# Kernel tuning notes

Measured on AMD Instinct MI355X. Metric: run time of the kernel, lower is better.

## Reference

```python
import jax, jax.numpy as jnp
import numpy as np

T, D, H = 8192, 128, 1024  # seq_len, obs_dim, lstm_hidden_size


def setup_inputs() -> dict:
    key = jax.random.key(0)
    ks = jax.random.split(key, 9)
    lim = 1.0 / np.sqrt(H)  # eqx LSTMCell/Linear uniform init scale

    def u(k, shape):
        return jax.random.uniform(k, shape, minval=-lim, maxval=lim, dtype=jnp.float32)

    obs = jax.random.normal(ks[0], (T, D), dtype=jnp.float32)
    W_ih0 = u(ks[1], (4 * H, D))
    W_hh0 = u(ks[2], (4 * H, H))
    b0 = u(ks[3], (4 * H,))
    W_ih1 = u(ks[4], (4 * H, H))
    W_hh1 = u(ks[5], (4 * H, H))
    b1 = u(ks[6], (4 * H,))
    W_dec = u(ks[7], (2 * D, H))
    b_dec = u(ks[8], (2 * D,))
    return {"obs": obs, "W_ih0": W_ih0, "W_hh0": W_hh0, "b0": b0,
            "W_ih1": W_ih1, "W_hh1": W_hh1, "b1": b1,
            "W_dec": W_dec, "b_dec": b_dec}


def _lstm_cell(gx, h, c, W_hh):
    # gx: (4H,) precomputed input projection + bias; h, c: (H,)
    z = gx + W_hh @ h
    i, f, g, o = jnp.split(z, 4)
    i = jax.nn.sigmoid(i)
    f = jax.nn.sigmoid(f)
    g = jnp.tanh(g)
    o = jax.nn.sigmoid(o)
    c_new = f * c + i * g
    h_new = o * jnp.tanh(c_new)
    return h_new, c_new


def reference(obs, W_ih0, W_hh0, b0, W_ih1, W_hh1, b1, W_dec, b_dec):
    d = obs.shape[1]
    hdim = W_hh0.shape[1]
    # teacher forcing: input at step t is obs[t-1], obs[-1] replaced by zeros
    shifted = jnp.concatenate([jnp.zeros((1, d), obs.dtype), obs[:-1]], axis=0)
    # layer-0 input projection is input-only -> precompute as one big GEMM (T, 4H)
    gx0_all = shifted @ W_ih0.T + b0

    def step(state, gx0_t):
        (h0, c0), (h1, c1) = state
        h0, c0 = _lstm_cell(gx0_t, h0, c0, W_hh0)
        gx1 = W_ih1 @ h0 + b1
        h1, c1 = _lstm_cell(gx1, h1, c1, W_hh1)
        return ((h0, c0), (h1, c1)), h1

    z = jnp.zeros((hdim,), obs.dtype)
    init = ((z, z), (z, z))
    _, all_h = jax.lax.scan(step, init, gx0_all)  # all_h: (T, H)

    params = all_h @ W_dec.T + b_dec  # (T, 2D)
    loc = params[:, :d]
    scale = jax.nn.softplus(params[:, d:]) + 1e-4
    return loc, scale
```

## Files before the change

### kernel.cpp

```cpp
#include <hip/hip_runtime.h>
#include <math.h>

#define TT 8192
#define DD 128
#define HH 1024
#define RINGN 64
#define NA 64
#define NB 128
#define NWG (NA + NB)


typedef unsigned long long ull;

__device__ __forceinline__ ull ldpair(const ull* p) {
  return __hip_atomic_load(p, __ATOMIC_RELAXED, __HIP_MEMORY_SCOPE_AGENT);
}
__device__ __forceinline__ void stpair(ull* p, float v, unsigned e) {
  ull u = ((ull)e << 32) | (ull)__float_as_uint(v);
  __hip_atomic_store(p, u, __ATOMIC_RELAXED, __HIP_MEMORY_SCOPE_AGENT);
}
__device__ __forceinline__ unsigned ldflag(const unsigned* p) {
  return __hip_atomic_load(p, __ATOMIC_RELAXED, __HIP_MEMORY_SCOPE_AGENT);
}
__device__ __forceinline__ void stflag(unsigned* p, unsigned v) {
  __hip_atomic_store(p, v, __ATOMIC_RELAXED, __HIP_MEMORY_SCOPE_AGENT);
}
__device__ __forceinline__ float sigm(float x) { return 1.0f / (1.0f + expf(-x)); }
__device__ __forceinline__ float softplusf(float x) {
  return x > 0.0f ? x + log1pf(expf(-x)) : log1pf(expf(x));
}

#define DRAIN()  asm volatile("s_waitcnt vmcnt(0)" ::: "memory")
#define CFENCE() asm volatile("" ::: "memory")

#define FMA16(W)                                                      \
  a0 = fmaf(W[0][4*i+0], h4.x, a0); a0 = fmaf(W[0][4*i+1], h4.y, a0); \
  a0 = fmaf(W[0][4*i+2], h4.z, a0); a0 = fmaf(W[0][4*i+3], h4.w, a0); \
  a1 = fmaf(W[1][4*i+0], h4.x, a1); a1 = fmaf(W[1][4*i+1], h4.y, a1); \
  a1 = fmaf(W[1][4*i+2], h4.z, a1); a1 = fmaf(W[1][4*i+3], h4.w, a1); \
  a2 = fmaf(W[2][4*i+0], h4.x, a2); a2 = fmaf(W[2][4*i+1], h4.y, a2); \
  a2 = fmaf(W[2][4*i+2], h4.z, a2); a2 = fmaf(W[2][4*i+3], h4.w, a2); \
  a3 = fmaf(W[3][4*i+0], h4.x, a3); a3 = fmaf(W[3][4*i+1], h4.y, a3); \
  a3 = fmaf(W[3][4*i+2], h4.z, a3); a3 = fmaf(W[3][4*i+3], h4.w, a3);

__global__ void __launch_bounds__(512, 1) deepar_persistent(
    const float* __restrict__ obs,
    const float* __restrict__ Wih0, const float* __restrict__ Whh0, const float* __restrict__ b0,
    const float* __restrict__ Wih1, const float* __restrict__ Whh1, const float* __restrict__ b1,
    const float* __restrict__ Wdec, const float* __restrict__ bdec,
    float* __restrict__ out,
    unsigned* b_cons, unsigned* a_fA, unsigned* a_fB, unsigned* b_fB,
    ull* h0A, ull* h0B, ull* h1B)
{
  __shared__ __align__(16) float hx[2][2304];

  const int wg   = blockIdx.x;
  const int tid  = threadIdx.x;
  const int wid  = tid >> 6;
  const int lane = tid & 63;

  if (wg < NA) {
    const int rg = tid >> 5;
    const int q  = tid & 31;
    const int j  = wg * 16 + rg;
    const int k0 = q * 36;
    float w[4][36];
    #pragma unroll
    for (int i = 0; i < 9; ++i) {
      const int kb = k0 + 4 * i;
      #pragma unroll
      for (int r = 0; r < 4; ++r) {
        const float* src = (kb < HH) ? (Whh0 + (size_t)(r * HH + j) * HH + kb)
                                     : (Wih0 + (size_t)(r * HH + j) * DD + (kb - HH));
        const float4 v = *(const float4*)src;
        w[r][4*i+0] = v.x; w[r][4*i+1] = v.y; w[r][4*i+2] = v.z; w[r][4*i+3] = v.w;
      }
    }
    float bs[4];
    #pragma unroll
    for (int r = 0; r < 4; ++r) bs[r] = b0[r * HH + j];
    float creg = 0.0f;

    for (int t = 0; t < TT; ++t) {
      float a0 = 0.f, a1 = 0.f, a2 = 0.f, a3 = 0.f;
      if (t > 0) {
        const float* obr = obs + (size_t)(t - 1) * DD;
        #pragma unroll
        for (int i = 0; i < 9; ++i) {
          const int kb = k0 + 4 * i;
          if (kb >= HH) { const float4 h4 = *(const float4*)(obr + (kb - HH)); FMA16(w) }
        }
      }
      if (wid == 1 && ((t & 15) == 0) && t >= 48) {
        const unsigned need = (unsigned)(t - 32);
        while (!__all((ldflag(&b_cons[lane]) >= need) &
                      (ldflag(&b_cons[lane + 64]) >= need))) {}
      }
      if (wid == 0 && t > 0) {
        const unsigned tg = (unsigned)t;
        while (!__all((lane == wg) | (ldflag(&a_fA[lane]) >= tg))) {}
      }
      __builtin_amdgcn_s_barrier();
      float* Lb = hx[t & 1];
      if (t > 0) {
        const ull* sl = h0A + (size_t)((t - 1) & (RINGN - 1)) * HH;
        const unsigned ee = (unsigned)t;
        ull u0 = ldpair(sl + tid);
        ull u1 = ldpair(sl + tid + 512);
        while ((unsigned)(u0 >> 32) != ee) u0 = ldpair(sl + tid);
        Lb[tid] = __uint_as_float((unsigned)u0);
        while ((unsigned)(u1 >> 32) != ee) u1 = ldpair(sl + tid + 512);
        Lb[tid + 512] = __uint_as_float((unsigned)u1);
      }
      __syncthreads();
      if (t > 0) {
        #pragma unroll
        for (int i = 0; i < 9; ++i) {
          const int kb = k0 + 4 * i;
          if (kb < HH) { const float4 h4 = *(const float4*)&Lb[kb]; FMA16(w) }
        }
      }
      #pragma unroll
      for (int s = 1; s < 32; s <<= 1) {
        a0 += __shfl_xor(a0, s); a1 += __shfl_xor(a1, s);
        a2 += __shfl_xor(a2, s); a3 += __shfl_xor(a3, s);
      }
      if (q == 0) {
        const float ig = sigm(a0 + bs[0]);
        const float fg = sigm(a1 + bs[1]);
        const float gg = tanhf(a2 + bs[2]);
        const float og = sigm(a3 + bs[3]);
        creg = fg * creg + ig * gg;
        const float hv = og * tanhf(creg);
        const size_t off = (size_t)(t & (RINGN - 1)) * HH + j;
        const unsigned ep = (unsigned)(t + 1);
        stpair(&h0A[off], hv, ep);
        stpair(&h0B[off], hv, ep);
      }
      DRAIN();
      __builtin_amdgcn_s_barrier();
      CFENCE();
      if (tid == 0) { stflag(&a_fA[wg], (unsigned)(t + 1));
                      stflag(&a_fB[wg], (unsigned)(t + 1)); }
    }

  } else {
    const int rg = tid >> 6;
    const int q  = tid & 63;
    const int s_ = wg - NA;
    const int j  = s_ * 8 + rg;
    const int k0 = q * 32;
    float w[4][32];
    #pragma unroll
    for (int i = 0; i < 8; ++i) {
      const int kb = k0 + 4 * i;
      #pragma unroll
      for (int r = 0; r < 4; ++r) {
        const float* src = (kb < HH) ? (Wih1 + (size_t)(r * HH + j) * HH + kb)
                                     : (Whh1 + (size_t)(r * HH + j) * HH + (kb - HH));
        const float4 v = *(const float4*)src;
        w[r][4*i+0] = v.x; w[r][4*i+1] = v.y; w[r][4*i+2] = v.z; w[r][4*i+3] = v.w;
      }
    }
    float bs[4];
    #pragma unroll
    for (int r = 0; r < 4; ++r) bs[r] = b1[r * HH + j];
    float creg = 0.0f;
    const int p0 = tid + 4 * (tid >> 5);
    const int p1 = p0 + 576;
    const int p2 = p0 + 1152;
    const int p3 = p2 + 576;
    const int baseB = (q < 32) ? q * 36 : 1152 + (q - 32) * 36;
    const int crow = s_ * 2 + (wid - 2);
    float wd[16];
    float bsd = 0.0f;
    if (wid == 2 || wid == 3) {
      #pragma unroll
      for (int i = 0; i < 4; ++i) {
        const float4 v = *(const float4*)(Wdec + (size_t)crow * HH + lane * 16 + 4 * i);
        wd[4*i+0] = v.x; wd[4*i+1] = v.y; wd[4*i+2] = v.z; wd[4*i+3] = v.w;
      }
      bsd = bdec[crow];
    }
    const int dbase = 1152 + lane * 16 + 4 * ((lane * 16) >> 5);

    for (int t = 0; t <= TT; ++t) {
      if (wid == 0) {
        const unsigned eA = (unsigned)(t + 1);
        const unsigned eB = (unsigned)t;
        for (;;) {
          int ok = 1;
          if (t < TT) ok &= (ldflag(&a_fB[lane]) >= eA);
          if (t > 0) {
            ok &= (lane == s_)        | (ldflag(&b_fB[lane])      >= eB);
            ok &= ((lane + 64) == s_) | (ldflag(&b_fB[lane + 64]) >= eB);
          }
          if (__all(ok)) break;
        }
      }
      __builtin_amdgcn_s_barrier();
      float* Lb = hx[t & 1];
      {
        const unsigned e0 = (unsigned)(t + 1);
        const unsigned e1 = (unsigned)t;
        if (t < TT) {
          const ull* s0 = h0B + (size_t)(t & (RINGN - 1)) * HH;
          ull u0 = ldpair(s0 + tid);
          ull u1 = ldpair(s0 + tid + 512);
          while ((unsigned)(u0 >> 32) != e0) u0 = ldpair(s0 + tid);
          Lb[p0] = __uint_as_float((unsigned)u0);
          while ((unsigned)(u1 >> 32) != e0) u1 = ldpair(s0 + tid + 512);
          Lb[p1] = __uint_as_float((unsigned)u1);
        }
        const ull* s1 = h1B + (size_t)((t - 1) & (RINGN - 1)) * HH;
        ull u2 = ldpair(s1 + tid);
        ull u3 = ldpair(s1 + tid + 512);
        while ((unsigned)(u2 >> 32) != e1) u2 = ldpair(s1 + tid);
        Lb[p2] = __uint_as_float((unsigned)u2);
        while ((unsigned)(u3 >> 32) != e1) u3 = ldpair(s1 + tid + 512);
        Lb[p3] = __uint_as_float((unsigned)u3);
      }
      __syncthreads();
      if (tid == 64 && t < TT) stflag(&b_cons[s_], (unsigned)(t + 1));
      if (t < TT) {
        float a0 = 0.f, a1 = 0.f, a2 = 0.f, a3 = 0.f;
        #pragma unroll
        for (int i = 0; i < 8; ++i) {
          const float4 h4 = *(const float4*)&Lb[baseB + 4 * i];
          FMA16(w)
        }
        #pragma unroll
        for (int s = 1; s < 64; s <<= 1) {
          a0 += __shfl_xor(a0, s); a1 += __shfl_xor(a1, s);
          a2 += __shfl_xor(a2, s); a3 += __shfl_xor(a3, s);
        }
        if (q == 0) {
          const float ig = sigm(a0 + bs[0]);
          const float fg = sigm(a1 + bs[1]);
          const float gg = tanhf(a2 + bs[2]);
          const float og = sigm(a3 + bs[3]);
          creg = fg * creg + ig * gg;
          stpair(&h1B[(size_t)(t & (RINGN - 1)) * HH + j], og * tanhf(creg),
                 (unsigned)(t + 1));
        }
        DRAIN();
        __builtin_amdgcn_s_barrier();
        CFENCE();
        if (tid == 0) stflag(&b_fB[s_], (unsigned)(t + 1));
      }
      if (t > 0 && (wid == 2 || wid == 3)) {
        float a = 0.f;
        #pragma unroll
        for (int i = 0; i < 4; ++i) {
          const float4 h4 = *(const float4*)&Lb[dbase + 4 * i];
          a = fmaf(wd[4*i+0], h4.x, a); a = fmaf(wd[4*i+1], h4.y, a);
          a = fmaf(wd[4*i+2], h4.z, a); a = fmaf(wd[4*i+3], h4.w, a);
        }
        #pragma unroll
        for (int s = 1; s < 64; s <<= 1) a += __shfl_xor(a, s);
        if (lane == 0) {
          const float z = a + bsd;
          if (crow < DD) out[(size_t)(t - 1) * DD + crow] = z;
          else out[(size_t)TT * DD + (size_t)(t - 1) * DD + (crow - DD)]
                 = softplusf(z) + 1e-4f;
        }
      }
    }
  }
}

extern "C" void kernel_launch(void* const* d_in, const int* in_sizes, int n_in,
                              void* d_out, int out_size, void* d_ws, size_t ws_size,
                              hipStream_t stream) {
  const float* obs  = (const float*)d_in[0];
  const float* Wih0 = (const float*)d_in[1];
  const float* Whh0 = (const float*)d_in[2];
  const float* b0   = (const float*)d_in[3];
  const float* Wih1 = (const float*)d_in[4];
  const float* Whh1 = (const float*)d_in[5];
  const float* b1   = (const float*)d_in[6];
  const float* Wdec = (const float*)d_in[7];
  const float* bdec = (const float*)d_in[8];
  float* out = (float*)d_out;

  const size_t RB = (size_t)RINGN * HH * 8;
  unsigned char* ws = (unsigned char*)d_ws;
  unsigned* b_cons = (unsigned*)(ws);
  unsigned* a_fA   = (unsigned*)(ws + 1024);
  unsigned* a_fB   = (unsigned*)(ws + 1536);
  unsigned* b_fB   = (unsigned*)(ws + 2048);
  ull* h0A = (ull*)(ws + 4096);
  ull* h0B = (ull*)(ws + 4096 + RB);
  ull* h1B = (ull*)(ws + 4096 + 2 * RB);

  hipMemsetAsync(ws, 0, 4096 + 3 * RB, stream);

  hipLaunchKernelGGL(deepar_persistent, dim3(NWG), dim3(512), 0, stream,
                     obs, Wih0, Whh0, b0, Wih1, Whh1, b1, Wdec, bdec, out,
                     b_cons, a_fA, a_fB, b_fB, h0A, h0B, h1B);
}
```

Measured before the change: 34.40 ms.

## Replace per-step flag barriers with epoch-tagged ring polling by a single wave

Drops the per-workgroup completion flags (a_fA, a_fB, b_fB) and the drain-plus-barrier that published them. Consumers now rely only on the epoch tags stored with each h value. One wave per workgroup sweeps the whole 1024-entry ring slot with 16 outstanding loads per lane and re-polls only the entries that are still stale. Layer-0 wave 0 defers its obs contribution until after the LDS barrier so the poll starts sooner. This removes a flag round-trip and a vmcnt drain from the recurrent critical path, but concentrates the polling traffic in one wave and leans on the per-element epoch checks alone for correctness.

```diff
diff --git a/kernel.cpp b/kernel.cpp
--- a/kernel.cpp
+++ b/kernel.cpp
@@ -30,8 +30,31 @@
   return x > 0.0f ? x + log1pf(expf(-x)) : log1pf(expf(x));
 }
 
-#define DRAIN()  asm volatile("s_waitcnt vmcnt(0)" ::: "memory")
-#define CFENCE() asm volatile("" ::: "memory")
+template<int PAD>
+__device__ __forceinline__ void sweep_ring(const ull* sl, unsigned ee,
+                                           float* lds, int lane) {
+  ull v[16];
+  #pragma unroll
+  for (int k = 0; k < 16; ++k) v[k] = ldpair(sl + lane + 64 * k);
+  unsigned pend = 0xFFFFu;
+  for (;;) {
+    unsigned np = 0u;
+    #pragma unroll
+    for (int k = 0; k < 16; ++k) {
+      if (pend & (1u << k)) {
+        if ((unsigned)(v[k] >> 32) == ee) {
+          const int m = lane + 64 * k;
+          lds[PAD ? (m + 4 * (m >> 5)) : m] = __uint_as_float((unsigned)v[k]);
+        } else np |= (1u << k);
+      }
+    }
+    if (!np) break;
+    pend = np;
+    #pragma unroll
+    for (int k = 0; k < 16; ++k)
+      if (pend & (1u << k)) v[k] = ldpair(sl + lane + 64 * k);
+  }
+}
 
 #define FMA16(W)                                                      \
   a0 = fmaf(W[0][4*i+0], h4.x, a0); a0 = fmaf(W[0][4*i+1], h4.y, a0); \
@@ -49,8 +72,7 @@
     const float* __restrict__ Wih1, const float* __restrict__ Whh1, const float* __restrict__ b1,
     const float* __restrict__ Wdec, const float* __restrict__ bdec,
     float* __restrict__ out,
-    unsigned* b_cons, unsigned* a_fA, unsigned* a_fB, unsigned* b_fB,
-    ull* h0A, ull* h0B, ull* h1B)
+    unsigned* b_cons, ull* h0A, ull* h0B, ull* h1B)
 {
   __shared__ __align__(16) float hx[2][2304];
 
@@ -83,7 +105,7 @@
 
     for (int t = 0; t < TT; ++t) {
       float a0 = 0.f, a1 = 0.f, a2 = 0.f, a3 = 0.f;
-      if (t > 0) {
+      if (wid != 0 && t > 0) {
         const float* obr = obs + (size_t)(t - 1) * DD;
         #pragma unroll
         for (int i = 0; i < 9; ++i) {
@@ -91,29 +113,25 @@
           if (kb >= HH) { const float4 h4 = *(const float4*)(obr + (kb - HH)); FMA16(w) }
         }
       }
-      if (wid == 1 && ((t & 15) == 0) && t >= 48) {
+      if (wid == 2 && ((t & 15) == 0) && t >= 48) {
         const unsigned need = (unsigned)(t - 32);
         while (!__all((ldflag(&b_cons[lane]) >= need) &
                       (ldflag(&b_cons[lane + 64]) >= need))) {}
       }
-      if (wid == 0 && t > 0) {
-        const unsigned tg = (unsigned)t;
-        while (!__all((lane == wg) | (ldflag(&a_fA[lane]) >= tg))) {}
-      }
-      __builtin_amdgcn_s_barrier();
       float* Lb = hx[t & 1];
-      if (t > 0) {
-        const ull* sl = h0A + (size_t)((t - 1) & (RINGN - 1)) * HH;
-        const unsigned ee = (unsigned)t;
-        ull u0 = ldpair(sl + tid);
-        ull u1 = ldpair(sl + tid + 512);
-        while ((unsigned)(u0 >> 32) != ee) u0 = ldpair(sl + tid);
-        Lb[tid] = __uint_as_float((unsigned)u0);
-        while ((unsigned)(u1 >> 32) != ee) u1 = ldpair(sl + tid + 512);
-        Lb[tid + 512] = __uint_as_float((unsigned)u1);
-      }
+      if (wid == 0 && t > 0)
+        sweep_ring<0>(h0A + (size_t)((t - 1) & (RINGN - 1)) * HH,
+                      (unsigned)t, Lb, lane);
       __syncthreads();
       if (t > 0) {
+        if (wid == 0) {
+          const float* obr = obs + (size_t)(t - 1) * DD;
+          #pragma unroll
+          for (int i = 0; i < 9; ++i) {
+            const int kb = k0 + 4 * i;
+            if (kb >= HH) { const float4 h4 = *(const float4*)(obr + (kb - HH)); FMA16(w) }
+          }
+        }
         #pragma unroll
         for (int i = 0; i < 9; ++i) {
           const int kb = k0 + 4 * i;
@@ -137,11 +155,6 @@
         stpair(&h0A[off], hv, ep);
         stpair(&h0B[off], hv, ep);
       }
-      DRAIN();
-      __builtin_amdgcn_s_barrier();
-      CFENCE();
-      if (tid == 0) { stflag(&a_fA[wg], (unsigned)(t + 1));
-                      stflag(&a_fB[wg], (unsigned)(t + 1)); }
     }
 
   } else {
@@ -166,62 +179,27 @@
     #pragma unroll
     for (int r = 0; r < 4; ++r) bs[r] = b1[r * HH + j];
     float creg = 0.0f;
-    const int p0 = tid + 4 * (tid >> 5);
-    const int p1 = p0 + 576;
-    const int p2 = p0 + 1152;
-    const int p3 = p2 + 576;
     const int baseB = (q < 32) ? q * 36 : 1152 + (q - 32) * 36;
     const int crow = s_ * 2 + (wid - 2);
     float wd[16];
     float bsd = 0.0f;
     if (wid == 2 || wid == 3) {
       #pragma unroll
-      for (int i = 0; i < 4; ++i) {
-        const float4 v = *(const float4*)(Wdec + (size_t)crow * HH + lane * 16 + 4 * i);
-        wd[4*i+0] = v.x; wd[4*i+1] = v.y; wd[4*i+2] = v.z; wd[4*i+3] = v.w;
-      }
+      for (int k = 0; k < 16; ++k)
+        wd[k] = Wdec[(size_t)crow * HH + lane + 64 * k];
       bsd = bdec[crow];
     }
-    const int dbase = 1152 + lane * 16 + 4 * ((lane * 16) >> 5);
 
     for (int t = 0; t <= TT; ++t) {
-      if (wid == 0) {
-        const unsigned eA = (unsigned)(t + 1);
-        const unsigned eB = (unsigned)t;
-        for (;;) {
-          int ok = 1;
-          if (t < TT) ok &= (ldflag(&a_fB[lane]) >= eA);
-          if (t > 0) {
-            ok &= (lane == s_)        | (ldflag(&b_fB[lane])      >= eB);
-            ok &= ((lane + 64) == s_) | (ldflag(&b_fB[lane + 64]) >= eB);
-          }
-          if (__all(ok)) break;
-        }
-      }
-      __builtin_amdgcn_s_barrier();
       float* Lb = hx[t & 1];
-      {
-        const unsigned e0 = (unsigned)(t + 1);
-        const unsigned e1 = (unsigned)t;
-        if (t < TT) {
-          const ull* s0 = h0B + (size_t)(t & (RINGN - 1)) * HH;
-          ull u0 = ldpair(s0 + tid);
-          ull u1 = ldpair(s0 + tid + 512);
-          while ((unsigned)(u0 >> 32) != e0) u0 = ldpair(s0 + tid);
-          Lb[p0] = __uint_as_float((unsigned)u0);
-          while ((unsigned)(u1 >> 32) != e0) u1 = ldpair(s0 + tid + 512);
-          Lb[p1] = __uint_as_float((unsigned)u1);
-        }
-        const ull* s1 = h1B + (size_t)((t - 1) & (RINGN - 1)) * HH;
-        ull u2 = ldpair(s1 + tid);
-        ull u3 = ldpair(s1 + tid + 512);
-        while ((unsigned)(u2 >> 32) != e1) u2 = ldpair(s1 + tid);
-        Lb[p2] = __uint_as_float((unsigned)u2);
-        while ((unsigned)(u3 >> 32) != e1) u3 = ldpair(s1 + tid + 512);
-        Lb[p3] = __uint_as_float((unsigned)u3);
-      }
+      if (wid == 0)
+        sweep_ring<1>(h1B + (size_t)((t - 1) & (RINGN - 1)) * HH,
+                      (unsigned)t, Lb + 1152, lane);
+      if (wid == 1 && t < TT)
+        sweep_ring<1>(h0B + (size_t)(t & (RINGN - 1)) * HH,
+                      (unsigned)(t + 1), Lb, lane);
       __syncthreads();
-      if (tid == 64 && t < TT) stflag(&b_cons[s_], (unsigned)(t + 1));
+      if (tid == 256 && t < TT) stflag(&b_cons[s_], (unsigned)(t + 1));
       if (t < TT) {
         float a0 = 0.f, a1 = 0.f, a2 = 0.f, a3 = 0.f;
         #pragma unroll
@@ -243,18 +221,13 @@
           stpair(&h1B[(size_t)(t & (RINGN - 1)) * HH + j], og * tanhf(creg),
                  (unsigned)(t + 1));
         }
-        DRAIN();
-        __builtin_amdgcn_s_barrier();
-        CFENCE();
-        if (tid == 0) stflag(&b_fB[s_], (unsigned)(t + 1));
       }
       if (t > 0 && (wid == 2 || wid == 3)) {
         float a = 0.f;
         #pragma unroll
-        for (int i = 0; i < 4; ++i) {
-          const float4 h4 = *(const float4*)&Lb[dbase + 4 * i];
-          a = fmaf(wd[4*i+0], h4.x, a); a = fmaf(wd[4*i+1], h4.y, a);
-          a = fmaf(wd[4*i+2], h4.z, a); a = fmaf(wd[4*i+3], h4.w, a);
+        for (int k = 0; k < 16; ++k) {
+          const int m = lane + 64 * k;
+          a = fmaf(wd[k], Lb[1152 + m + 4 * (m >> 5)], a);
         }
         #pragma unroll
         for (int s = 1; s < 64; s <<= 1) a += __shfl_xor(a, s);
@@ -286,9 +259,6 @@
   const size_t RB = (size_t)RINGN * HH * 8;
   unsigned char* ws = (unsigned char*)d_ws;
   unsigned* b_cons = (unsigned*)(ws);
-  unsigned* a_fA   = (unsigned*)(ws + 1024);
-  unsigned* a_fB   = (unsigned*)(ws + 1536);
-  unsigned* b_fB   = (unsigned*)(ws + 2048);
   ull* h0A = (ull*)(ws + 4096);
   ull* h0B = (ull*)(ws + 4096 + RB);
   ull* h1B = (ull*)(ws + 4096 + 2 * RB);
@@ -297,5 +267,5 @@
 
   hipLaunchKernelGGL(deepar_persistent, dim3(NWG), dim3(512), 0, stream,
                      obs, Wih0, Whh0, b0, Wih1, Whh1, b1, Wdec, bdec, out,
-                     b_cons, a_fA, a_fB, b_fB, h0A, h0B, h1B);
-}
+                     b_cons, h0A, h0B, h1B);
+}
```

Result: slower. 55.86 ms (+62.4%).

## Drop per-step flag barriers, replicate hidden-state rings across eight copies

Applied to the files above, without the earlier changes.

Removes the per-workgroup completion flags and the drain-plus-barrier handshake. Consumers now wait only on the epoch-tagged value pairs, so each step needs no separate flag round trip. Each h value is written to eight replicated ring buffers so readers spread across copies instead of contending on one, and the ring depth drops to 32 with a tighter backpressure window. The decoder weight layout changes to a lane-strided form. The risks are an eightfold increase in store traffic per step and a narrower margin against ring wraparound.

```diff
diff --git a/kernel.cpp b/kernel.cpp
--- a/kernel.cpp
+++ b/kernel.cpp
@@ -4,10 +4,12 @@
 #define TT 8192
 #define DD 128
 #define HH 1024
-#define RINGN 64
+#define RINGN 32
+#define NREP 8
 #define NA 64
 #define NB 128
 #define NWG (NA + NB)
+#define RSTRIDE ((size_t)RINGN * HH)
 
 
 typedef unsigned long long ull;
@@ -15,8 +17,7 @@
 __device__ __forceinline__ ull ldpair(const ull* p) {
   return __hip_atomic_load(p, __ATOMIC_RELAXED, __HIP_MEMORY_SCOPE_AGENT);
 }
-__device__ __forceinline__ void stpair(ull* p, float v, unsigned e) {
-  ull u = ((ull)e << 32) | (ull)__float_as_uint(v);
+__device__ __forceinline__ void stpair(ull* p, ull u) {
   __hip_atomic_store(p, u, __ATOMIC_RELAXED, __HIP_MEMORY_SCOPE_AGENT);
 }
 __device__ __forceinline__ unsigned ldflag(const unsigned* p) {
@@ -29,9 +30,6 @@
 __device__ __forceinline__ float softplusf(float x) {
   return x > 0.0f ? x + log1pf(expf(-x)) : log1pf(expf(x));
 }
-
-#define DRAIN()  asm volatile("s_waitcnt vmcnt(0)" ::: "memory")
-#define CFENCE() asm volatile("" ::: "memory")
 
 #define FMA16(W)                                                      \
   a0 = fmaf(W[0][4*i+0], h4.x, a0); a0 = fmaf(W[0][4*i+1], h4.y, a0); \
@@ -49,8 +47,7 @@
     const float* __restrict__ Wih1, const float* __restrict__ Whh1, const float* __restrict__ b1,
     const float* __restrict__ Wdec, const float* __restrict__ bdec,
     float* __restrict__ out,
-    unsigned* b_cons, unsigned* a_fA, unsigned* a_fB, unsigned* b_fB,
-    ull* h0A, ull* h0B, ull* h1B)
+    unsigned* b_cons, ull* h0R, ull* h1R)
 {
   __shared__ __align__(16) float hx[2][2304];
 
@@ -80,33 +77,27 @@
     #pragma unroll
     for (int r = 0; r < 4; ++r) bs[r] = b0[r * HH + j];
     float creg = 0.0f;
+    const ull* myrep = h0R + (size_t)(wg & 7) * RSTRIDE;
 
     for (int t = 0; t < TT; ++t) {
+      if (wid == 2 && ((t & 7) == 0) && t >= 24) {
+        const unsigned need = (unsigned)(t - 16);
+        while (!__all((ldflag(&b_cons[lane]) >= need) &
+                      (ldflag(&b_cons[lane + 64]) >= need))) {}
+      }
       float a0 = 0.f, a1 = 0.f, a2 = 0.f, a3 = 0.f;
+      float* Lb = hx[t & 1];
       if (t > 0) {
+        const ull* sl = myrep + (size_t)((t - 1) & (RINGN - 1)) * HH;
+        ull u0 = ldpair(sl + tid);
+        ull u1 = ldpair(sl + tid + 512);
         const float* obr = obs + (size_t)(t - 1) * DD;
         #pragma unroll
         for (int i = 0; i < 9; ++i) {
           const int kb = k0 + 4 * i;
           if (kb >= HH) { const float4 h4 = *(const float4*)(obr + (kb - HH)); FMA16(w) }
         }
-      }
-      if (wid == 1 && ((t & 15) == 0) && t >= 48) {
-        const unsigned need = (unsigned)(t - 32);
-        while (!__all((ldflag(&b_cons[lane]) >= need) &
-                      (ldflag(&b_cons[lane + 64]) >= need))) {}
-      }
-      if (wid == 0 && t > 0) {
-        const unsigned tg = (unsigned)t;
-        while (!__all((lane == wg) | (ldflag(&a_fA[lane]) >= tg))) {}
-      }
-      __builtin_amdgcn_s_barrier();
-      float* Lb = hx[t & 1];
-      if (t > 0) {
-        const ull* sl = h0A + (size_t)((t - 1) & (RINGN - 1)) * HH;
         const unsigned ee = (unsigned)t;
-        ull u0 = ldpair(sl + tid);
-        ull u1 = ldpair(sl + tid + 512);
         while ((unsigned)(u0 >> 32) != ee) u0 = ldpair(sl + tid);
         Lb[tid] = __uint_as_float((unsigned)u0);
         while ((unsigned)(u1 >> 32) != ee) u1 = ldpair(sl + tid + 512);
@@ -133,15 +124,11 @@
         creg = fg * creg + ig * gg;
         const float hv = og * tanhf(creg);
         const size_t off = (size_t)(t & (RINGN - 1)) * HH + j;
-        const unsigned ep = (unsigned)(t + 1);
-        stpair(&h0A[off], hv, ep);
-        stpair(&h0B[off], hv, ep);
-      }
-      DRAIN();
-      __builtin_amdgcn_s_barrier();
-      CFENCE();
-      if (tid == 0) { stflag(&a_fA[wg], (unsigned)(t + 1));
-                      stflag(&a_fB[wg], (unsigned)(t + 1)); }
+        const ull u = ((ull)(unsigned)(t + 1) << 32) | (ull)__float_as_uint(hv);
+        #pragma unroll
+        for (int r = 0; r < NREP; ++r)
+          stpair(h0R + (size_t)r * RSTRIDE + off, u);
+      }
     }
 
   } else {
@@ -171,40 +158,28 @@
     const int p2 = p0 + 1152;
     const int p3 = p2 + 576;
     const int baseB = (q < 32) ? q * 36 : 1152 + (q - 32) * 36;
+    const ull* rep0 = h0R + (size_t)(s_ & 7) * RSTRIDE;
+    const ull* rep1 = h1R + (size_t)(s_ & 7) * RSTRIDE;
     const int crow = s_ * 2 + (wid - 2);
     float wd[16];
     float bsd = 0.0f;
     if (wid == 2 || wid == 3) {
       #pragma unroll
-      for (int i = 0; i < 4; ++i) {
-        const float4 v = *(const float4*)(Wdec + (size_t)crow * HH + lane * 16 + 4 * i);
-        wd[4*i+0] = v.x; wd[4*i+1] = v.y; wd[4*i+2] = v.z; wd[4*i+3] = v.w;
-      }
+      for (int k = 0; k < 16; ++k)
+        wd[k] = Wdec[(size_t)crow * HH + lane + 64 * k];
       bsd = bdec[crow];
     }
-    const int dbase = 1152 + lane * 16 + 4 * ((lane * 16) >> 5);
 
     for (int t = 0; t <= TT; ++t) {
-      if (wid == 0) {
-        const unsigned eA = (unsigned)(t + 1);
-        const unsigned eB = (unsigned)t;
-        for (;;) {
-          int ok = 1;
-          if (t < TT) ok &= (ldflag(&a_fB[lane]) >= eA);
-          if (t > 0) {
-            ok &= (lane == s_)        | (ldflag(&b_fB[lane])      >= eB);
-            ok &= ((lane + 64) == s_) | (ldflag(&b_fB[lane + 64]) >= eB);
-          }
-          if (__all(ok)) break;
-        }
-      }
-      __builtin_amdgcn_s_barrier();
       float* Lb = hx[t & 1];
       {
         const unsigned e0 = (unsigned)(t + 1);
         const unsigned e1 = (unsigned)t;
+        const ull* s1 = rep1 + (size_t)((t - 1) & (RINGN - 1)) * HH;
+        ull u2 = ldpair(s1 + tid);
+        ull u3 = ldpair(s1 + tid + 512);
         if (t < TT) {
-          const ull* s0 = h0B + (size_t)(t & (RINGN - 1)) * HH;
+          const ull* s0 = rep0 + (size_t)(t & (RINGN - 1)) * HH;
           ull u0 = ldpair(s0 + tid);
           ull u1 = ldpair(s0 + tid + 512);
           while ((unsigned)(u0 >> 32) != e0) u0 = ldpair(s0 + tid);
@@ -212,16 +187,13 @@
           while ((unsigned)(u1 >> 32) != e0) u1 = ldpair(s0 + tid + 512);
           Lb[p1] = __uint_as_float((unsigned)u1);
         }
-        const ull* s1 = h1B + (size_t)((t - 1) & (RINGN - 1)) * HH;
-        ull u2 = ldpair(s1 + tid);
-        ull u3 = ldpair(s1 + tid + 512);
         while ((unsigned)(u2 >> 32) != e1) u2 = ldpair(s1 + tid);
         Lb[p2] = __uint_as_float((unsigned)u2);
         while ((unsigned)(u3 >> 32) != e1) u3 = ldpair(s1 + tid + 512);
         Lb[p3] = __uint_as_float((unsigned)u3);
       }
       __syncthreads();
-      if (tid == 64 && t < TT) stflag(&b_cons[s_], (unsigned)(t + 1));
+      if (tid == 256 && t < TT) stflag(&b_cons[s_], (unsigned)(t + 1));
       if (t < TT) {
         float a0 = 0.f, a1 = 0.f, a2 = 0.f, a3 = 0.f;
         #pragma unroll
@@ -240,21 +212,20 @@
           const float gg = tanhf(a2 + bs[2]);
           const float og = sigm(a3 + bs[3]);
           creg = fg * creg + ig * gg;
-          stpair(&h1B[(size_t)(t & (RINGN - 1)) * HH + j], og * tanhf(creg),
-                 (unsigned)(t + 1));
-        }
-        DRAIN();
-        __builtin_amdgcn_s_barrier();
-        CFENCE();
-        if (tid == 0) stflag(&b_fB[s_], (unsigned)(t + 1));
+          const float hv = og * tanhf(creg);
+          const size_t off = (size_t)(t & (RINGN - 1)) * HH + j;
+          const ull u = ((ull)(unsigned)(t + 1) << 32) | (ull)__float_as_uint(hv);
+          #pragma unroll
+          for (int r = 0; r < NREP; ++r)
+            stpair(h1R + (size_t)r * RSTRIDE + off, u);
+        }
       }
       if (t > 0 && (wid == 2 || wid == 3)) {
         float a = 0.f;
         #pragma unroll
-        for (int i = 0; i < 4; ++i) {
-          const float4 h4 = *(const float4*)&Lb[dbase + 4 * i];
-          a = fmaf(wd[4*i+0], h4.x, a); a = fmaf(wd[4*i+1], h4.y, a);
-          a = fmaf(wd[4*i+2], h4.z, a); a = fmaf(wd[4*i+3], h4.w, a);
+        for (int k = 0; k < 16; ++k) {
+          const int m = lane + 64 * k;
+          a = fmaf(wd[k], Lb[1152 + m + 4 * (m >> 5)], a);
         }
         #pragma unroll
         for (int s = 1; s < 64; s <<= 1) a += __shfl_xor(a, s);
@@ -286,16 +257,12 @@
   const size_t RB = (size_t)RINGN * HH * 8;
   unsigned char* ws = (unsigned char*)d_ws;
   unsigned* b_cons = (unsigned*)(ws);
-  unsigned* a_fA   = (unsigned*)(ws + 1024);
-  unsigned* a_fB   = (unsigned*)(ws + 1536);
-  unsigned* b_fB   = (unsigned*)(ws + 2048);
-  ull* h0A = (ull*)(ws + 4096);
-  ull* h0B = (ull*)(ws + 4096 + RB);
-  ull* h1B = (ull*)(ws + 4096 + 2 * RB);
-
-  hipMemsetAsync(ws, 0, 4096 + 3 * RB, stream);
+  ull* h0R = (ull*)(ws + 8192);
+  ull* h1R = (ull*)(ws + 8192 + NREP * RB);
+
+  hipMemsetAsync(ws, 0, 8192 + (size_t)2 * NREP * RB, stream);
 
   hipLaunchKernelGGL(deepar_persistent, dim3(NWG), dim3(512), 0, stream,
                      obs, Wih0, Whh0, b0, Wih1, Whh1, b1, Wdec, bdec, out,
-                     b_cons, a_fA, a_fB, b_fB, h0A, h0B, h1B);
-}
+                     b_cons, h0R, h1R);
+}
```

Measured after the change: 34.42 ms. About the same (+0.1%).
